# Kernel tuning notes

Measured on AMD Instinct MI355X. Metric: run time of the kernel, lower is better.

## Reference

```python
import jax, jax.numpy as jnp
import numpy as np

D_MODEL = 512
NUM_HEADS = 8
D_K = D_MODEL // NUM_HEADS


def setup_inputs() -> dict:
    key = jax.random.key(0)
    ks = jax.random.split(key, 9)
    B, N = 4, 2048
    x = jax.random.normal(ks[0], (B, N, D_MODEL), dtype=jnp.float32)
    s = 1.0 / np.sqrt(D_MODEL)
    Wq = jax.random.normal(ks[1], (D_MODEL, D_MODEL), dtype=jnp.float32) * s
    bq = jax.random.normal(ks[2], (D_MODEL,), dtype=jnp.float32) * 0.02
    Wk = jax.random.normal(ks[3], (D_MODEL, D_MODEL), dtype=jnp.float32) * s
    bk = jax.random.normal(ks[4], (D_MODEL,), dtype=jnp.float32) * 0.02
    Wv = jax.random.normal(ks[5], (D_MODEL, D_MODEL), dtype=jnp.float32) * s
    bv = jax.random.normal(ks[6], (D_MODEL,), dtype=jnp.float32) * 0.02
    Wo = jax.random.normal(ks[7], (D_MODEL, D_MODEL), dtype=jnp.float32) * s
    bo = jax.random.normal(ks[8], (D_MODEL,), dtype=jnp.float32) * 0.02
    return {"x": x, "Wq": Wq, "bq": bq, "Wk": Wk, "bk": bk,
            "Wv": Wv, "bv": bv, "Wo": Wo, "bo": bo}


def reference(x, Wq, bq, Wk, bk, Wv, bv, Wo, bo):
    B, N, _ = x.shape
    # project and split heads: [B, H, N, d_k]
    def split_heads(t):
        return t.reshape(B, N, NUM_HEADS, D_K).transpose(0, 2, 1, 3)
    Q = split_heads(x @ Wq + bq)
    K = split_heads(x @ Wk + bk)
    V = split_heads(x @ Wv + bv)
    scale = 1.0 / np.sqrt(D_K)
    scores = jnp.einsum('bhqd,bhkd->bhqk', Q, K) * scale  # [B,H,N,N]
    probs = jax.nn.softmax(scores, axis=-1)
    attn = jnp.einsum('bhqk,bhkd->bhqd', probs, V)
    attn = attn.transpose(0, 2, 1, 3).reshape(B, N, D_MODEL)
    return attn @ Wo + bo
```

## Files before the change

kernel.cpp:

```cpp
#include <hip/hip_runtime.h>
#include <math.h>

#define D_MODEL 512
#define N_SEQ   2048
#define H       8
#define DK      64
#define NQT     (N_SEQ / 128)

typedef __attribute__((ext_vector_type(8)))  short bf16x8;
typedef __attribute__((ext_vector_type(4)))  float f32x4;
typedef __attribute__((ext_vector_type(16))) float f32x16;

__device__ __forceinline__ unsigned short f2b(float f) {
    unsigned int u = __float_as_uint(f);
    u += 0x7FFF + ((u >> 16) & 1);
    return (unsigned short)(u >> 16);
}

__device__ __forceinline__ unsigned int pack2(float lo, float hi) {
#if __has_builtin(__builtin_amdgcn_cvt_pk_bf16_f32)
    typedef __attribute__((ext_vector_type(2))) short bf16x2;
    bf16x2 p = __builtin_amdgcn_cvt_pk_bf16_f32(lo, hi);
    return (unsigned int)(unsigned short)p[0] |
           ((unsigned int)(unsigned short)p[1] << 16);
#else
    return (unsigned int)f2b(lo) | ((unsigned int)f2b(hi) << 16);
#endif
}

__device__ __forceinline__ float fexp2(float x) {
#if __has_builtin(__builtin_amdgcn_exp2f)
    return __builtin_amdgcn_exp2f(x);
#else
    return __expf(x * 0.6931471805599453f);
#endif
}

#define SC2 0.18033688011112042f

__global__ void transpose_all(
    const float* __restrict__ W0, const float* __restrict__ W1,
    const float* __restrict__ W2, const float* __restrict__ W3,
    unsigned short* __restrict__ T0, unsigned short* __restrict__ T1,
    unsigned short* __restrict__ T2, unsigned short* __restrict__ T3)
{
    const float* W; unsigned short* Wt;
    if      (blockIdx.z == 0) { W = W0; Wt = T0; }
    else if (blockIdx.z == 1) { W = W1; Wt = T1; }
    else if (blockIdx.z == 2) { W = W2; Wt = T2; }
    else                      { W = W3; Wt = T3; }

    __shared__ float t[32][33];
    const int tx = threadIdx.x, ty = threadIdx.y;
    const int x = blockIdx.x * 32 + tx;
    const int y0 = blockIdx.y * 32;
    for (int i = ty; i < 32; i += 8)
        t[i][tx] = W[(size_t)(y0 + i) * D_MODEL + x];
    __syncthreads();
    const int ox = blockIdx.y * 32 + tx;
    const int oy0 = blockIdx.x * 32;
    for (int i = ty; i < 32; i += 8)
        Wt[(size_t)(oy0 + i) * D_MODEL + ox] = f2b(t[tx][i]);
}

template<int AMODE, int SWAP>
__device__ __forceinline__ void gemm_body(
    const void* __restrict__ Aptr,
    const unsigned short* __restrict__ Wt,
    const float* __restrict__ bias,
    void* __restrict__ out, int mode, int bx, int by, float sc,
    unsigned short (*As)[72], unsigned short (*Bs)[72])
{
    const int tid  = threadIdx.x;
    const int lane = tid & 63, wave = tid >> 6;
    const int m0 = by * 128, n0 = bx * 128;
    const int wm = (wave & 1) * 64, wn = (wave >> 1) * 64;
    const int cn = lane & 15, g = lane >> 4;

    const int srow = tid >> 1;
    const int scol = (tid & 1) * 32;
    const float* Agf = (const float*)Aptr + (size_t)(m0 + srow) * D_MODEL + scol;
    const unsigned short* Agb =
        (const unsigned short*)Aptr + (size_t)(m0 + srow) * D_MODEL + scol;
    const unsigned short* Bg = Wt + (size_t)(n0 + srow) * D_MODEL + scol;

    f32x4 acc[4][4];
    #pragma unroll
    for (int i = 0; i < 4; ++i)
        #pragma unroll
        for (int j = 0; j < 4; ++j)
            acc[i][j] = (f32x4){0.f, 0.f, 0.f, 0.f};

    for (int k0 = 0; k0 < D_MODEL; k0 += 64) {
        bf16x8 av[4], bv[4];
        #pragma unroll
        for (int q = 0; q < 4; ++q) {
            if (AMODE) {
                float4 f0 = *(const float4*)(Agf + k0 + q * 8);
                float4 f1 = *(const float4*)(Agf + k0 + q * 8 + 4);
                unsigned int* pv = (unsigned int*)&av[q];
                pv[0] = pack2(f0.x, f0.y); pv[1] = pack2(f0.z, f0.w);
                pv[2] = pack2(f1.x, f1.y); pv[3] = pack2(f1.z, f1.w);
            } else {
                av[q] = *(const bf16x8*)(Agb + k0 + q * 8);
            }
            bv[q] = *(const bf16x8*)(Bg + k0 + q * 8);
        }
        __syncthreads();
        #pragma unroll
        for (int q = 0; q < 4; ++q) {
            *(bf16x8*)&As[srow][scol + q * 8] = av[q];
            *(bf16x8*)&Bs[srow][scol + q * 8] = bv[q];
        }
        __syncthreads();

        #pragma unroll
        for (int ks = 0; ks < 2; ++ks) {
            bf16x8 af[4], bf[4];
            #pragma unroll
            for (int i = 0; i < 4; ++i)
                af[i] = *(const bf16x8*)&As[wm + i * 16 + cn][ks * 32 + g * 8];
            #pragma unroll
            for (int j = 0; j < 4; ++j)
                bf[j] = *(const bf16x8*)&Bs[wn + j * 16 + cn][ks * 32 + g * 8];
            #pragma unroll
            for (int i = 0; i < 4; ++i)
                #pragma unroll
                for (int j = 0; j < 4; ++j) {
                    if (SWAP)
                        acc[i][j] = __builtin_amdgcn_mfma_f32_16x16x32_bf16(
                            bf[j], af[i], acc[i][j], 0, 0, 0);
                    else
                        acc[i][j] = __builtin_amdgcn_mfma_f32_16x16x32_bf16(
                            af[i], bf[j], acc[i][j], 0, 0, 0);
                }
        }
    }

    if constexpr (SWAP) {
        unsigned short* o = (unsigned short*)out;
        #pragma unroll
        for (int j = 0; j < 4; ++j) {
            const int dbase = n0 + wn + j * 16 + g * 4;
            const int hh = dbase >> 6, dd = dbase & 63;
            float4 bb = *(const float4*)&bias[dbase];
            #pragma unroll
            for (int i = 0; i < 4; ++i) {
                const int tt = m0 + wm + i * 16 + cn;
                const int bi = tt >> 11, tok = tt & (N_SEQ - 1);
                ushort4 pk;
                pk.x = f2b((acc[i][j][0] + bb.x) * sc);
                pk.y = f2b((acc[i][j][1] + bb.y) * sc);
                pk.z = f2b((acc[i][j][2] + bb.z) * sc);
                pk.w = f2b((acc[i][j][3] + bb.w) * sc);
                *(ushort4*)(o + (((size_t)bi * H + hh) * N_SEQ + tok) * DK + dd) = pk;
            }
        }
    } else {
        unsigned short* o = (unsigned short*)out;
        #pragma unroll
        for (int j = 0; j < 4; ++j) {
            const int n = n0 + wn + j * 16 + cn;
            const int h = n >> 6, d = n & 63;
            const float bb = bias[n];
            #pragma unroll
            for (int i = 0; i < 4; ++i) {
                const int m = m0 + wm + i * 16 + g * 4;
                const int b = m >> 11, t = m & (N_SEQ - 1);
                ushort4 pk;
                pk.x = f2b(acc[i][j][0] + bb);
                pk.y = f2b(acc[i][j][1] + bb);
                pk.z = f2b(acc[i][j][2] + bb);
                pk.w = f2b(acc[i][j][3] + bb);
                *(ushort4*)(o + (((size_t)b * H + h) * DK + d) * N_SEQ + t) = pk;
            }
        }
    }
    (void)mode;
}

__global__ __launch_bounds__(256, 4) void gemm_qkv(
    const float* __restrict__ x,
    const unsigned short* __restrict__ Wtq,
    const unsigned short* __restrict__ Wtk,
    const unsigned short* __restrict__ Wtv,
    const float* __restrict__ bq, const float* __restrict__ bk,
    const float* __restrict__ bv,
    unsigned short* __restrict__ Qb, unsigned short* __restrict__ Kb,
    unsigned short* __restrict__ Vtb)
{
    __shared__ unsigned short As[128][72];
    __shared__ unsigned short Bs[128][72];
    if (blockIdx.z == 0)
        gemm_body<1, 1>(x, Wtq, bq, Qb, 0, blockIdx.x, blockIdx.y, SC2, As, Bs);
    else if (blockIdx.z == 1)
        gemm_body<1, 1>(x, Wtk, bk, Kb, 0, blockIdx.x, blockIdx.y, 1.0f, As, Bs);
    else
        gemm_body<1, 0>(x, Wtv, bv, Vtb, 1, blockIdx.x, blockIdx.y, 1.0f, As, Bs);
}

__global__ __launch_bounds__(256, 4) void gemm_o(
    const unsigned short* __restrict__ A,
    const unsigned short* __restrict__ Wt,
    const float* __restrict__ bias, float* __restrict__ out)
{
    __shared__ unsigned short As[64][72];
    __shared__ unsigned short Bs[64][72];

    const int tid  = threadIdx.x;
    const int lane = tid & 63, wave = tid >> 6;
    const int m0 = blockIdx.y * 64, n0 = blockIdx.x * 64;
    const int wm = (wave & 1) * 32, wn = (wave >> 1) * 32;
    const int cn = lane & 15, g = lane >> 4;

    const int srow = tid >> 2;
    const int scol = (tid & 3) * 16;
    const unsigned short* Ag = A  + (size_t)(m0 + srow) * D_MODEL + scol;
    const unsigned short* Bg = Wt + (size_t)(n0 + srow) * D_MODEL + scol;

    f32x4 acc[2][2];
    #pragma unroll
    for (int i = 0; i < 2; ++i)
        #pragma unroll
        for (int j = 0; j < 2; ++j)
            acc[i][j] = (f32x4){0.f, 0.f, 0.f, 0.f};

    for (int k0 = 0; k0 < D_MODEL; k0 += 64) {
        bf16x8 av[2], bv[2];
        #pragma unroll
        for (int q = 0; q < 2; ++q) {
            av[q] = *(const bf16x8*)(Ag + k0 + q * 8);
            bv[q] = *(const bf16x8*)(Bg + k0 + q * 8);
        }
        __syncthreads();
        #pragma unroll
        for (int q = 0; q < 2; ++q) {
            *(bf16x8*)&As[srow][scol + q * 8] = av[q];
            *(bf16x8*)&Bs[srow][scol + q * 8] = bv[q];
        }
        __syncthreads();

        #pragma unroll
        for (int ks = 0; ks < 2; ++ks) {
            bf16x8 af[2], bf[2];
            #pragma unroll
            for (int i = 0; i < 2; ++i)
                af[i] = *(const bf16x8*)&As[wm + i * 16 + cn][ks * 32 + g * 8];
            #pragma unroll
            for (int j = 0; j < 2; ++j)
                bf[j] = *(const bf16x8*)&Bs[wn + j * 16 + cn][ks * 32 + g * 8];
            #pragma unroll
            for (int i = 0; i < 2; ++i)
                #pragma unroll
                for (int j = 0; j < 2; ++j)
                    acc[i][j] = __builtin_amdgcn_mfma_f32_16x16x32_bf16(
                        af[i], bf[j], acc[i][j], 0, 0, 0);
        }
    }

    #pragma unroll
    for (int j = 0; j < 2; ++j) {
        const int n = n0 + wn + j * 16 + cn;
        const float bb = bias[n];
        #pragma unroll
        for (int i = 0; i < 2; ++i)
            #pragma unroll
            for (int r = 0; r < 4; ++r) {
                const int m = m0 + wm + i * 16 + g * 4 + r;
                out[(size_t)m * D_MODEL + n] = acc[i][j][r] + bb;
            }
    }
}

__global__ __launch_bounds__(512, 4) void attn_mfma(
    const unsigned short* __restrict__ Q,
    const unsigned short* __restrict__ K,
    const unsigned short* __restrict__ Vt,
    unsigned short* __restrict__ ctx)
{
    __shared__ unsigned short SM[2][2][64][72];

    const int tid = threadIdx.x, lane = tid & 63, wave = tid >> 6;
    const int qt = blockIdx.x, h = blockIdx.y, b = blockIdx.z;
    const int sp = wave >> 2;
    const int w4 = wave & 3;
    const int lq = lane & 31, hf = lane >> 5;
    const int q0 = qt * 128;
    const int qs = q0 + w4 * 32;

    const size_t hb = (size_t)b * H + h;
    const unsigned short* Qp = Q  + hb * N_SEQ * DK;
    const unsigned short* Kp = K  + hb * N_SEQ * DK;
    const unsigned short* Vp = Vt + hb * DK * N_SEQ;

    bf16x8 qf[4];
    #pragma unroll
    for (int kd = 0; kd < 4; ++kd)
        qf[kd] = *(const bf16x8*)(Qp + (size_t)(qs + lq) * DK + kd * 16 + hf * 8);

    f32x16 O[2], Ol;
    #pragma unroll
    for (int r = 0; r < 16; ++r) { O[0][r] = 0.f; O[1][r] = 0.f; Ol[r] = 0.f; }

    bf16x8 onesA;
    {
        const short v = (lq == 0) ? (short)0x3F80 : (short)0;
        #pragma unroll
        for (int j = 0; j < 8; ++j) onesA[j] = v;
    }

    const int tl = tid & 255;
    const int krow = tl >> 2, kcol = (tl & 3) * 16;
    unsigned short (*Ks)[72] = SM[sp][0];
    unsigned short (*Vs)[72] = SM[sp][1];

    for (int it = 0; it < 16; ++it) {
        const int j0 = sp * (N_SEQ / 2) + it * 64;
        bf16x8 kv0 = *(const bf16x8*)(Kp + (size_t)(j0 + krow) * DK + kcol);
        bf16x8 kv1 = *(const bf16x8*)(Kp + (size_t)(j0 + krow) * DK + kcol + 8);
        bf16x8 vv0 = *(const bf16x8*)(Vp + (size_t)krow * N_SEQ + j0 + kcol);
        bf16x8 vv1 = *(const bf16x8*)(Vp + (size_t)krow * N_SEQ + j0 + kcol + 8);
        bf16x8 sw0, sw1;
        {
            ushort4* a = (ushort4*)&vv0;
            ushort4* c = (ushort4*)&vv1;
            ushort4* s0p = (ushort4*)&sw0;
            ushort4* s1p = (ushort4*)&sw1;
            s0p[0] = a[0]; s0p[1] = c[0];
            s1p[0] = a[1]; s1p[1] = c[1];
        }
        __syncthreads();
        *(bf16x8*)&Ks[krow][kcol]     = kv0;
        *(bf16x8*)&Ks[krow][kcol + 8] = kv1;
        *(bf16x8*)&Vs[krow][kcol]     = sw0;
        *(bf16x8*)&Vs[krow][kcol + 8] = sw1;
        __syncthreads();

        f32x16 s0, s1;
        #pragma unroll
        for (int r = 0; r < 16; ++r) { s0[r] = 0.f; s1[r] = 0.f; }
        #pragma unroll
        for (int kd = 0; kd < 4; ++kd) {
            bf16x8 a0 = *(const bf16x8*)&Ks[lq][kd * 16 + hf * 8];
            bf16x8 a1 = *(const bf16x8*)&Ks[32 + lq][kd * 16 + hf * 8];
            s0 = __builtin_amdgcn_mfma_f32_32x32x16_bf16(a0, qf[kd], s0, 0, 0, 0);
            s1 = __builtin_amdgcn_mfma_f32_32x32x16_bf16(a1, qf[kd], s1, 0, 0, 0);
        }

        unsigned int pk0[4][2], pk1[4][2];
        #pragma unroll
        for (int c = 0; c < 4; ++c)
            #pragma unroll
            for (int p = 0; p < 2; ++p) {
                pk0[c][p] = pack2(fexp2(s0[4 * c + 2 * p]),
                                  fexp2(s0[4 * c + 2 * p + 1]));
                pk1[c][p] = pack2(fexp2(s1[4 * c + 2 * p]),
                                  fexp2(s1[4 * c + 2 * p + 1]));
            }

        #pragma unroll
        for (int ks = 0; ks < 4; ++ks) {
            const unsigned int (*src)[2] = (ks < 2) ? pk0 : pk1;
            const int c2 = (ks & 1) * 2;
            bf16x8 bp;
            unsigned int* bpu = (unsigned int*)&bp;
            bpu[0] = src[c2][0];     bpu[1] = src[c2][1];
            bpu[2] = src[c2 + 1][0]; bpu[3] = src[c2 + 1][1];
            bf16x8 va0 = *(const bf16x8*)&Vs[lq][ks * 16 + hf * 8];
            bf16x8 va1 = *(const bf16x8*)&Vs[32 + lq][ks * 16 + hf * 8];
            O[0] = __builtin_amdgcn_mfma_f32_32x32x16_bf16(va0, bp, O[0], 0, 0, 0);
            O[1] = __builtin_amdgcn_mfma_f32_32x32x16_bf16(va1, bp, O[1], 0, 0, 0);
            Ol   = __builtin_amdgcn_mfma_f32_32x32x16_bf16(onesA, bp, Ol, 0, 0, 0);
        }
    }

    float* R    = (float*)&SM[0][0][0][0];
    float* Laux = R + 4 * 64 * 32;

    __syncthreads();
    if (sp == 1) {
        #pragma unroll
        for (int dt = 0; dt < 2; ++dt)
            #pragma unroll
            for (int r = 0; r < 16; ++r) {
                const int d = (r & 3) + 8 * (r >> 2) + 4 * hf + 32 * dt;
                R[(w4 * 64 + d) * 32 + lq] = O[dt][r];
            }
        if (hf == 0) Laux[w4 * 32 + lq] = Ol[0];
    }
    __syncthreads();
    if (sp == 0) {
        #pragma unroll
        for (int dt = 0; dt < 2; ++dt)
            #pragma unroll
            for (int r = 0; r < 16; ++r) {
                const int d = (r & 3) + 8 * (r >> 2) + 4 * hf + 32 * dt;
                O[dt][r] += R[(w4 * 64 + d) * 32 + lq];
            }
        const float lsum = Ol[0] + Laux[w4 * 32 + lq];
        const float linv = 1.0f / __shfl(lsum, lq);

        unsigned short* ob = ctx + ((size_t)b * N_SEQ + qs + lq) * D_MODEL
                                 + h * DK + hf * 4;
        #pragma unroll
        for (int dt = 0; dt < 2; ++dt)
            #pragma unroll
            for (int c = 0; c < 4; ++c) {
                unsigned int w2[2];
                w2[0] = pack2(O[dt][4 * c + 0] * linv, O[dt][4 * c + 1] * linv);
                w2[1] = pack2(O[dt][4 * c + 2] * linv, O[dt][4 * c + 3] * linv);
                *(unsigned int*)(ob + dt * 32 + c * 8)     = w2[0];
                *(unsigned int*)(ob + dt * 32 + c * 8 + 2) = w2[1];
            }
    }
}

extern "C" void kernel_launch(void* const* d_in, const int* in_sizes, int n_in,
                              void* d_out, int out_size, void* d_ws, size_t ws_size,
                              hipStream_t stream)
{
    const float* x  = (const float*)d_in[0];
    const float* Wq = (const float*)d_in[1];
    const float* bq = (const float*)d_in[2];
    const float* Wk = (const float*)d_in[3];
    const float* bk = (const float*)d_in[4];
    const float* Wv = (const float*)d_in[5];
    const float* bv = (const float*)d_in[6];
    const float* Wo = (const float*)d_in[7];
    const float* bo = (const float*)d_in[8];
    float* out = (float*)d_out;

    const int M = in_sizes[0] / D_MODEL;
    const int nb = M / N_SEQ;
    const size_t NX = (size_t)M * D_MODEL;
    const size_t NW = (size_t)D_MODEL * D_MODEL;

    unsigned short* Wtq = (unsigned short*)d_ws;
    unsigned short* Wtk = Wtq + NW;
    unsigned short* Wtv = Wtk + NW;
    unsigned short* Wto = Wtv + NW;
    unsigned short* Qb  = Wto + NW;
    unsigned short* Kb  = Qb + NX;
    unsigned short* Vtb = Kb + NX;
    unsigned short* ctx = Vtb + NX;

    transpose_all<<<dim3(16, 16, 4), dim3(32, 8), 0, stream>>>(
        Wq, Wk, Wv, Wo, Wtq, Wtk, Wtv, Wto);

    gemm_qkv<<<dim3(D_MODEL / 128, M / 128, 3), 256, 0, stream>>>(
        x, Wtq, Wtk, Wtv, bq, bk, bv, Qb, Kb, Vtb);
    attn_mfma<<<dim3(NQT, H, nb), 512, 0, stream>>>(Qb, Kb, Vtb, ctx);
    gemm_o<<<dim3(D_MODEL / 64, M / 64), 256, 0, stream>>>(ctx, Wto, bo, out);
}
```

Measured before the change: 185.2 us.

## Pre-convert x to bf16, shrink QKV tiles, halve attention block size with remapped grid

Adds a separate pass that converts x to bf16 once, so the QKV GEMM no longer converts fp32 to bf16 three times inside its loads. The QKV GEMM tile drops from 128x128 to 128x64, doubling its block count. The attention kernel moves from 512-thread blocks over 128 queries to 256-thread blocks over 64 queries, using a 1D grid remapped so consecutive blocks span different heads and batches. This gives more, smaller blocks for occupancy and load balance, in exchange for an extra launch, a bf16 copy of x in workspace, and K/V tiles being reloaded by twice as many attention blocks.

```diff
diff --git a/kernel.cpp b/kernel.cpp
--- a/kernel.cpp
+++ b/kernel.cpp
@@ -5,7 +5,6 @@
 #define N_SEQ   2048
 #define H       8
 #define DK      64
-#define NQT     (N_SEQ / 128)
 
 typedef __attribute__((ext_vector_type(8)))  short bf16x8;
 typedef __attribute__((ext_vector_type(4)))  float f32x4;
@@ -37,6 +36,18 @@
 }
 
 #define SC2 0.18033688011112042f
+
+__global__ void convert_bf16(const float* __restrict__ in,
+                             unsigned short* __restrict__ out)
+{
+    const int i = (blockIdx.x * 256 + threadIdx.x) * 8;
+    float4 a = *(const float4*)(in + i);
+    float4 b = *(const float4*)(in + i + 4);
+    unsigned int w[4];
+    w[0] = pack2(a.x, a.y); w[1] = pack2(a.z, a.w);
+    w[2] = pack2(b.x, b.y); w[3] = pack2(b.z, b.w);
+    *(bf16x8*)(out + i) = *(bf16x8*)w;
+}
 
 __global__ void transpose_all(
     const float* __restrict__ W0, const float* __restrict__ W1,
@@ -63,84 +74,86 @@
         Wt[(size_t)(oy0 + i) * D_MODEL + ox] = f2b(t[tx][i]);
 }
 
-template<int AMODE, int SWAP>
-__device__ __forceinline__ void gemm_body(
-    const void* __restrict__ Aptr,
-    const unsigned short* __restrict__ Wt,
-    const float* __restrict__ bias,
-    void* __restrict__ out, int mode, int bx, int by, float sc,
-    unsigned short (*As)[72], unsigned short (*Bs)[72])
-{
+__global__ __launch_bounds__(256, 4) void gemm_qkv(
+    const unsigned short* __restrict__ xb,
+    const unsigned short* __restrict__ Wtq,
+    const unsigned short* __restrict__ Wtk,
+    const unsigned short* __restrict__ Wtv,
+    const float* __restrict__ bq, const float* __restrict__ bk,
+    const float* __restrict__ bv,
+    unsigned short* __restrict__ Qb, unsigned short* __restrict__ Kb,
+    unsigned short* __restrict__ Vtb)
+{
+    __shared__ unsigned short As[128][72];
+    __shared__ unsigned short Bs[64][72];
+
+    const unsigned short* Wt; const float* bias; unsigned short* out; int isV;
+    float sc;
+    if (blockIdx.z == 0)      { Wt = Wtq; bias = bq; out = Qb;  isV = 0; sc = SC2; }
+    else if (blockIdx.z == 1) { Wt = Wtk; bias = bk; out = Kb;  isV = 0; sc = 1.0f; }
+    else                      { Wt = Wtv; bias = bv; out = Vtb; isV = 1; sc = 1.0f; }
+
     const int tid  = threadIdx.x;
     const int lane = tid & 63, wave = tid >> 6;
-    const int m0 = by * 128, n0 = bx * 128;
-    const int wm = (wave & 1) * 64, wn = (wave >> 1) * 64;
+    const int m0 = blockIdx.y * 128, n0 = blockIdx.x * 64;
+    const int wm = (wave & 1) * 64, wn = (wave >> 1) * 32;
     const int cn = lane & 15, g = lane >> 4;
 
-    const int srow = tid >> 1;
-    const int scol = (tid & 1) * 32;
-    const float* Agf = (const float*)Aptr + (size_t)(m0 + srow) * D_MODEL + scol;
-    const unsigned short* Agb =
-        (const unsigned short*)Aptr + (size_t)(m0 + srow) * D_MODEL + scol;
-    const unsigned short* Bg = Wt + (size_t)(n0 + srow) * D_MODEL + scol;
-
-    f32x4 acc[4][4];
+    const int arow = tid >> 1, acol = (tid & 1) * 32;
+    const int brow = tid >> 2, bcol = (tid & 3) * 16;
+    const unsigned short* Ag = xb + (size_t)(m0 + arow) * D_MODEL + acol;
+    const unsigned short* Bg = Wt + (size_t)(n0 + brow) * D_MODEL + bcol;
+
+    f32x4 acc[4][2];
     #pragma unroll
     for (int i = 0; i < 4; ++i)
         #pragma unroll
-        for (int j = 0; j < 4; ++j)
+        for (int j = 0; j < 2; ++j)
             acc[i][j] = (f32x4){0.f, 0.f, 0.f, 0.f};
 
     for (int k0 = 0; k0 < D_MODEL; k0 += 64) {
-        bf16x8 av[4], bv[4];
-        #pragma unroll
-        for (int q = 0; q < 4; ++q) {
-            if (AMODE) {
-                float4 f0 = *(const float4*)(Agf + k0 + q * 8);
-                float4 f1 = *(const float4*)(Agf + k0 + q * 8 + 4);
-                unsigned int* pv = (unsigned int*)&av[q];
-                pv[0] = pack2(f0.x, f0.y); pv[1] = pack2(f0.z, f0.w);
-                pv[2] = pack2(f1.x, f1.y); pv[3] = pack2(f1.z, f1.w);
-            } else {
-                av[q] = *(const bf16x8*)(Agb + k0 + q * 8);
-            }
-            bv[q] = *(const bf16x8*)(Bg + k0 + q * 8);
-        }
-        __syncthreads();
-        #pragma unroll
-        for (int q = 0; q < 4; ++q) {
-            *(bf16x8*)&As[srow][scol + q * 8] = av[q];
-            *(bf16x8*)&Bs[srow][scol + q * 8] = bv[q];
-        }
+        bf16x8 av[4], bv2[2];
+        #pragma unroll
+        for (int q = 0; q < 4; ++q) av[q] = *(const bf16x8*)(Ag + k0 + q * 8);
+        #pragma unroll
+        for (int q = 0; q < 2; ++q) bv2[q] = *(const bf16x8*)(Bg + k0 + q * 8);
+        __syncthreads();
+        #pragma unroll
+        for (int q = 0; q < 4; ++q) *(bf16x8*)&As[arow][acol + q * 8] = av[q];
+        #pragma unroll
+        for (int q = 0; q < 2; ++q) *(bf16x8*)&Bs[brow][bcol + q * 8] = bv2[q];
         __syncthreads();
 
         #pragma unroll
         for (int ks = 0; ks < 2; ++ks) {
-            bf16x8 af[4], bf[4];
+            bf16x8 af[4], bf[2];
             #pragma unroll
             for (int i = 0; i < 4; ++i)
                 af[i] = *(const bf16x8*)&As[wm + i * 16 + cn][ks * 32 + g * 8];
             #pragma unroll
-            for (int j = 0; j < 4; ++j)
+            for (int j = 0; j < 2; ++j)
                 bf[j] = *(const bf16x8*)&Bs[wn + j * 16 + cn][ks * 32 + g * 8];
-            #pragma unroll
-            for (int i = 0; i < 4; ++i)
+            if (!isV) {
                 #pragma unroll
-                for (int j = 0; j < 4; ++j) {
-                    if (SWAP)
+                for (int i = 0; i < 4; ++i)
+                    #pragma unroll
+                    for (int j = 0; j < 2; ++j)
                         acc[i][j] = __builtin_amdgcn_mfma_f32_16x16x32_bf16(
                             bf[j], af[i], acc[i][j], 0, 0, 0);
-                    else
+            } else {
+                #pragma unroll
+                for (int i = 0; i < 4; ++i)
+                    #pragma unroll
+                    for (int j = 0; j < 2; ++j)
                         acc[i][j] = __builtin_amdgcn_mfma_f32_16x16x32_bf16(
                             af[i], bf[j], acc[i][j], 0, 0, 0);
-                }
-        }
-    }
-
-    if constexpr (SWAP) {
-        unsigned short* o = (unsigned short*)out;
-        #pragma unroll
-        for (int j = 0; j < 4; ++j) {
+            }
+        }
+    }
+
+    if (!isV) {
+        #pragma unroll
+        for (int j = 0; j < 2; ++j) {
             const int dbase = n0 + wn + j * 16 + g * 4;
             const int hh = dbase >> 6, dd = dbase & 63;
             float4 bb = *(const float4*)&bias[dbase];
@@ -153,50 +166,28 @@
                 pk.y = f2b((acc[i][j][1] + bb.y) * sc);
                 pk.z = f2b((acc[i][j][2] + bb.z) * sc);
                 pk.w = f2b((acc[i][j][3] + bb.w) * sc);
-                *(ushort4*)(o + (((size_t)bi * H + hh) * N_SEQ + tok) * DK + dd) = pk;
+                *(ushort4*)(out + (((size_t)bi * H + hh) * N_SEQ + tok) * DK + dd) = pk;
             }
         }
     } else {
-        unsigned short* o = (unsigned short*)out;
-        #pragma unroll
-        for (int j = 0; j < 4; ++j) {
+        #pragma unroll
+        for (int j = 0; j < 2; ++j) {
             const int n = n0 + wn + j * 16 + cn;
-            const int h = n >> 6, d = n & 63;
+            const int hh = n >> 6, dd = n & 63;
             const float bb = bias[n];
             #pragma unroll
             for (int i = 0; i < 4; ++i) {
                 const int m = m0 + wm + i * 16 + g * 4;
-                const int b = m >> 11, t = m & (N_SEQ - 1);
+                const int bi = m >> 11, t = m & (N_SEQ - 1);
                 ushort4 pk;
                 pk.x = f2b(acc[i][j][0] + bb);
                 pk.y = f2b(acc[i][j][1] + bb);
                 pk.z = f2b(acc[i][j][2] + bb);
                 pk.w = f2b(acc[i][j][3] + bb);
-                *(ushort4*)(o + (((size_t)b * H + h) * DK + d) * N_SEQ + t) = pk;
-            }
-        }
-    }
-    (void)mode;
-}
-
-__global__ __launch_bounds__(256, 4) void gemm_qkv(
-    const float* __restrict__ x,
-    const unsigned short* __restrict__ Wtq,
-    const unsigned short* __restrict__ Wtk,
-    const unsigned short* __restrict__ Wtv,
-    const float* __restrict__ bq, const float* __restrict__ bk,
-    const float* __restrict__ bv,
-    unsigned short* __restrict__ Qb, unsigned short* __restrict__ Kb,
-    unsigned short* __restrict__ Vtb)
-{
-    __shared__ unsigned short As[128][72];
-    __shared__ unsigned short Bs[128][72];
-    if (blockIdx.z == 0)
-        gemm_body<1, 1>(x, Wtq, bq, Qb, 0, blockIdx.x, blockIdx.y, SC2, As, Bs);
-    else if (blockIdx.z == 1)
-        gemm_body<1, 1>(x, Wtk, bk, Kb, 0, blockIdx.x, blockIdx.y, 1.0f, As, Bs);
-    else
-        gemm_body<1, 0>(x, Wtv, bv, Vtb, 1, blockIdx.x, blockIdx.y, 1.0f, As, Bs);
+                *(ushort4*)(out + (((size_t)bi * H + hh) * DK + dd) * N_SEQ + t) = pk;
+            }
+        }
+    }
 }
 
 __global__ __launch_bounds__(256, 4) void gemm_o(
@@ -272,7 +263,7 @@
     }
 }
 
-__global__ __launch_bounds__(512, 4) void attn_mfma(
+__global__ __launch_bounds__(256, 4) void attn_mfma(
     const unsigned short* __restrict__ Q,
     const unsigned short* __restrict__ K,
     const unsigned short* __restrict__ Vt,
@@ -280,13 +271,16 @@
 {
     __shared__ unsigned short SM[2][2][64][72];
 
+    const int bid = blockIdx.x;
+    const int qt = (bid >> 3) & 31;
+    const int bh = (bid & 7) * 4 + (bid >> 8);
+    const int b = bh >> 3, h = bh & 7;
+
     const int tid = threadIdx.x, lane = tid & 63, wave = tid >> 6;
-    const int qt = blockIdx.x, h = blockIdx.y, b = blockIdx.z;
-    const int sp = wave >> 2;
-    const int w4 = wave & 3;
+    const int sp = wave >> 1;
+    const int w4 = wave & 1;
     const int lq = lane & 31, hf = lane >> 5;
-    const int q0 = qt * 128;
-    const int qs = q0 + w4 * 32;
+    const int qs = qt * 64 + w4 * 32;
 
     const size_t hb = (size_t)b * H + h;
     const unsigned short* Qp = Q  + hb * N_SEQ * DK;
@@ -309,31 +303,39 @@
         for (int j = 0; j < 8; ++j) onesA[j] = v;
     }
 
-    const int tl = tid & 255;
-    const int krow = tl >> 2, kcol = (tl & 3) * 16;
-    unsigned short (*Ks)[72] = SM[sp][0];
-    unsigned short (*Vs)[72] = SM[sp][1];
+    const int sps = tid >> 7;
+    const int tl = tid & 127;
+    const int krow = tl >> 1, kcol = (tl & 1) * 32;
+    unsigned short (*Kss)[72] = SM[sps][0];
+    unsigned short (*Vss)[72] = SM[sps][1];
+    unsigned short (*Ks)[72]  = SM[sp][0];
+    unsigned short (*Vs)[72]  = SM[sp][1];
 
     for (int it = 0; it < 16; ++it) {
-        const int j0 = sp * (N_SEQ / 2) + it * 64;
-        bf16x8 kv0 = *(const bf16x8*)(Kp + (size_t)(j0 + krow) * DK + kcol);
-        bf16x8 kv1 = *(const bf16x8*)(Kp + (size_t)(j0 + krow) * DK + kcol + 8);
-        bf16x8 vv0 = *(const bf16x8*)(Vp + (size_t)krow * N_SEQ + j0 + kcol);
-        bf16x8 vv1 = *(const bf16x8*)(Vp + (size_t)krow * N_SEQ + j0 + kcol + 8);
-        bf16x8 sw0, sw1;
+        const int j0 = sps * (N_SEQ / 2) + it * 64;
+        bf16x8 kv[4], vv[4];
+        #pragma unroll
+        for (int q = 0; q < 4; ++q) {
+            kv[q] = *(const bf16x8*)(Kp + (size_t)(j0 + krow) * DK + kcol + q * 8);
+            vv[q] = *(const bf16x8*)(Vp + (size_t)krow * N_SEQ + j0 + kcol + q * 8);
+        }
+        bf16x8 sw[4];
         {
-            ushort4* a = (ushort4*)&vv0;
-            ushort4* c = (ushort4*)&vv1;
-            ushort4* s0p = (ushort4*)&sw0;
-            ushort4* s1p = (ushort4*)&sw1;
-            s0p[0] = a[0]; s0p[1] = c[0];
-            s1p[0] = a[1]; s1p[1] = c[1];
-        }
-        __syncthreads();
-        *(bf16x8*)&Ks[krow][kcol]     = kv0;
-        *(bf16x8*)&Ks[krow][kcol + 8] = kv1;
-        *(bf16x8*)&Vs[krow][kcol]     = sw0;
-        *(bf16x8*)&Vs[krow][kcol + 8] = sw1;
+            ushort4* v0 = (ushort4*)&vv[0]; ushort4* v1 = (ushort4*)&vv[1];
+            ushort4* v2 = (ushort4*)&vv[2]; ushort4* v3 = (ushort4*)&vv[3];
+            ushort4* s0 = (ushort4*)&sw[0]; ushort4* s1 = (ushort4*)&sw[1];
+            ushort4* s2 = (ushort4*)&sw[2]; ushort4* s3 = (ushort4*)&sw[3];
+            s0[0] = v0[0]; s0[1] = v1[0];
+            s1[0] = v0[1]; s1[1] = v1[1];
+            s2[0] = v2[0]; s2[1] = v3[0];
+            s3[0] = v2[1]; s3[1] = v3[1];
+        }
+        __syncthreads();
+        #pragma unroll
+        for (int q = 0; q < 4; ++q) {
+            *(bf16x8*)&Kss[krow][kcol + q * 8] = kv[q];
+            *(bf16x8*)&Vss[krow][kcol + q * 8] = sw[q];
+        }
         __syncthreads();
 
         f32x16 s0, s1;
@@ -375,7 +377,7 @@
     }
 
     float* R    = (float*)&SM[0][0][0][0];
-    float* Laux = R + 4 * 64 * 32;
+    float* Laux = R + 2 * 64 * 32;
 
     __syncthreads();
     if (sp == 1) {
@@ -431,11 +433,11 @@
     float* out = (float*)d_out;
 
     const int M = in_sizes[0] / D_MODEL;
-    const int nb = M / N_SEQ;
     const size_t NX = (size_t)M * D_MODEL;
     const size_t NW = (size_t)D_MODEL * D_MODEL;
 
-    unsigned short* Wtq = (unsigned short*)d_ws;
+    unsigned short* xb  = (unsigned short*)d_ws;
+    unsigned short* Wtq = xb + NX;
     unsigned short* Wtk = Wtq + NW;
     unsigned short* Wtv = Wtk + NW;
     unsigned short* Wto = Wtv + NW;
@@ -444,11 +446,12 @@
     unsigned short* Vtb = Kb + NX;
     unsigned short* ctx = Vtb + NX;
 
+    convert_bf16<<<NX / (256 * 8), 256, 0, stream>>>(x, xb);
     transpose_all<<<dim3(16, 16, 4), dim3(32, 8), 0, stream>>>(
         Wq, Wk, Wv, Wo, Wtq, Wtk, Wtv, Wto);
 
-    gemm_qkv<<<dim3(D_MODEL / 128, M / 128, 3), 256, 0, stream>>>(
-        x, Wtq, Wtk, Wtv, bq, bk, bv, Qb, Kb, Vtb);
-    attn_mfma<<<dim3(NQT, H, nb), 512, 0, stream>>>(Qb, Kb, Vtb, ctx);
+    gemm_qkv<<<dim3(D_MODEL / 64, M / 128, 3), 256, 0, stream>>>(
+        xb, Wtq, Wtk, Wtv, bq, bk, bv, Qb, Kb, Vtb);
+    attn_mfma<<<1024, 256, 0, stream>>>(Qb, Kb, Vtb, ctx);
     gemm_o<<<dim3(D_MODEL / 64, M / 64), 256, 0, stream>>>(ctx, Wto, bo, out);
 }
```

Measured after the change: 185.5 us. Within noise of the previous version (+0.2%).
